# Performance work log

Measured on AMD Instinct MI355X. Metric: run time of the kernel, lower is better.

The kernel has to match this reference:

```python
import jax, jax.numpy as jnp
import numpy as np
from jax import lax

EPS = 1e-12


def _conv_block(x, w, scale, bias, pool):
    # x: (N, Cin, H, W), w: (Cout, Cin, 3, 3). BN in eval mode folded into scale/bias.
    y = lax.conv_general_dilated(x, w, window_strides=(1, 1), padding='SAME',
                                 dimension_numbers=('NCHW', 'OIHW', 'NCHW'))
    y = y * scale[None, :, None, None] + bias[None, :, None, None]
    y = jax.nn.relu(y)
    if pool:
        y = lax.reduce_window(y, -jnp.inf, lax.max, (1, 1, 2, 2), (1, 1, 2, 2), 'VALID')
    return y


def _encoder(x, w1, s1, b1, w2, s2, b2, w3, s3, b3, w4, s4, b4):
    x = _conv_block(x, w1, s1, b1, True)
    x = _conv_block(x, w2, s2, b2, True)
    x = _conv_block(x, w3, s3, b3, False)
    x = _conv_block(x, w4, s4, b4, False)
    return x  # (N, 64, 21, 21)


def _l2norm(x, axis):
    n = jnp.sqrt(jnp.sum(x * x, axis=axis, keepdims=True))
    return x / jnp.maximum(n, EPS)


def setup_inputs() -> dict:
    key = jax.random.key(0)
    ks = jax.random.split(key, 8)
    B, NQ, Way, Shot, C, H, W = 2, 75, 5, 5, 3, 84, 84
    D = 64
    inp = {
        'query': jax.random.normal(ks[0], (B, NQ, C, H, W), jnp.float32),
        'support': jax.random.normal(ks[1], (B, Way, Shot, C, H, W), jnp.float32),
        'w1': jax.random.normal(ks[2], (D, C, 3, 3), jnp.float32) * 0.1,
        'w2': jax.random.normal(ks[3], (D, D, 3, 3), jnp.float32) * 0.05,
        'w3': jax.random.normal(ks[4], (D, D, 3, 3), jnp.float32) * 0.05,
        'w4': jax.random.normal(ks[5], (D, D, 3, 3), jnp.float32) * 0.05,
    }
    for i in range(1, 5):
        inp[f's{i}'] = jnp.ones((D,), jnp.float32)
        inp[f'b{i}'] = jnp.zeros((D,), jnp.float32)
    return inp


def reference(query, support, w1, s1, b1, w2, s2, b2, w3, s3, b3, w4, s4, b4):
    B, NQ, C, H, W = query.shape
    _, Way, Shot, _, _, _ = support.shape
    q_flat = query.reshape(B * NQ, C, H, W)
    s_flat = support.reshape(B * Way * Shot, C, H, W)
    q_feat = _encoder(q_flat, w1, s1, b1, w2, s2, b2, w3, s3, b3, w4, s4, b4)
    s_feat = _encoder(s_flat, w1, s1, b1, w2, s2, b2, w3, s3, b3, w4, s4, b4)
    D, h, w = q_feat.shape[1], q_feat.shape[2], q_feat.shape[3]
    HW = h * w
    q_local = _l2norm(q_feat.reshape(B, NQ, D, HW), axis=2)            # (B,NQ,D,HW)
    s_local = s_feat.reshape(B, Way, Shot, D, HW).mean(axis=2)          # mean over shots
    s_local = _l2norm(s_local, axis=2)                                  # (B,Way,D,HW)
    # all pairwise local cosine similarities, batched in one einsum
    sim = jnp.einsum('bqdm,bcdn->bqcmn', q_local, s_local)              # (B,NQ,Way,HW,HW)
    best = sim.max(axis=-1)                                             # best match per query descriptor
    scores = best.mean(axis=-1)                                         # (B,NQ,Way)
    return scores.reshape(B * NQ, Way)
```

## Files before the change

kernel.cpp:

```cpp
#include <hip/hip_runtime.h>

#define EPS 1e-12f

#define NIMG   200
#define NQIMG  150
#define BDIM   2
#define NQ     75
#define WAY    5
#define SHOT   5
#define DCH    64
#define H1     84
#define H2     42
#define H3     21
#define HW1    7056
#define HW2    1764
#define HW3    441
#define PH     86
#define PSZ    7396
#define SST    448

#define PAD_BLKS  17335
#define W1_BLKS   8
#define W_BLKS    432

typedef __attribute__((ext_vector_type(8))) short bf16x8;
typedef __attribute__((ext_vector_type(4))) float f32x4;

__device__ __forceinline__ unsigned short f2bf(float f) {
    unsigned u = __float_as_uint(f);
    u += 0x7fffu + ((u >> 16) & 1u);
    return (unsigned short)(u >> 16);
}
__device__ __forceinline__ float bf2f(unsigned short h) {
    return __uint_as_float(((unsigned)h) << 16);
}
__device__ __forceinline__ int swz(int pix, int c) {
    return pix * 128 + ((c ^ ((pix >> 1) & 7)) << 4);
}

__global__ __launch_bounds__(256) void prep(
    const float* __restrict__ qin, const float* __restrict__ sin_,
    const float* __restrict__ w1, const float* __restrict__ s1,
    const float* __restrict__ w2, const float* __restrict__ s2,
    const float* __restrict__ w3, const float* __restrict__ s3,
    const float* __restrict__ w4, const float* __restrict__ s4,
    unsigned short* __restrict__ pad, unsigned short* __restrict__ p1,
    unsigned short* __restrict__ p2, unsigned short* __restrict__ p3,
    unsigned short* __restrict__ p4)
{
    int blk = blockIdx.x;
    if (blk < PAD_BLKS) {
        int idx = blk * 256 + threadIdx.x;
        if (idx >= NIMG * 3 * PSZ) return;
        int img = idx / (3 * PSZ);
        int rem = idx % (3 * PSZ);
        int ci = rem / PSZ, p = rem % PSZ;
        int iy = p / PH, ix = p % PH;
        float v = 0.f;
        if (iy >= 1 && iy <= H1 && ix >= 1 && ix <= H1) {
            const float* src = (img < NQIMG) ? (qin + (size_t)img * 3 * HW1)
                                             : (sin_ + (size_t)(img - NQIMG) * 3 * HW1);
            v = src[(size_t)ci * HW1 + (iy - 1) * H1 + (ix - 1)];
        }
        pad[idx] = f2bf(v);
    } else if (blk < PAD_BLKS + W1_BLKS) {
        int idx = (blk - PAD_BLKS) * 256 + threadIdx.x;
        int j = idx & 7, lane = (idx >> 3) & 63, mt = idx >> 9;
        int co = (mt << 4) + (lane & 15);
        int k = ((lane >> 4) << 3) + j;
        float v = 0.f;
        if (k < 27) {
            int ci = k / 9, s = k % 9;
            v = w1[(co * 3 + ci) * 9 + s] * s1[co];
        }
        p1[idx] = f2bf(v);
    } else {
        int idx = (blk - PAD_BLKS - W1_BLKS) * 256 + threadIdx.x;
        int which = idx / 36864;
        int r = idx % 36864;
        int j = r & 7, lane = (r >> 3) & 63, mt = (r >> 9) & 3, t = (r >> 11) & 1, s = r >> 12;
        int co = (mt << 4) + (lane & 15);
        int ci = (t << 5) + ((lane >> 4) << 3) + j;
        const float* w = (which == 0) ? w2 : (which == 1) ? w3 : w4;
        const float* sc = (which == 0) ? s2 : (which == 1) ? s3 : s4;
        unsigned short* p = (which == 0) ? p2 : (which == 1) ? p3 : p4;
        p[r] = f2bf(w[(co * 64 + ci) * 9 + s] * sc[co]);
    }
}

__global__ __launch_bounds__(256) void conv1_mfma(
    const unsigned short* __restrict__ pad,
    const unsigned short* __restrict__ wp1,
    const float* __restrict__ bias,
    unsigned short* __restrict__ out)
{
    int img = blockIdx.x / 7, seg = blockIdx.x % 7;
    int tid = threadIdx.x;
    __shared__ unsigned short strip[3 * 14 * 86];

    const unsigned* srcd = (const unsigned*)pad;
    size_t ibase = (size_t)img * 3 * (PSZ / 2);
    #pragma unroll
    for (int it = 0; it < 8; it++) {
        int i = it * 256 + tid;
        if (i < 1806) {
            int ci = i / 602, r = i % 602;
            ((unsigned*)strip)[i] = srcd[ibase + ci * (PSZ / 2) + 516 * seg + r];
        }
    }
    __syncthreads();

    int wv = tid >> 6, lane = tid & 63;
    int lc = lane & 15, kg = lane >> 4;

    const bf16x8* wvv = (const bf16x8*)wp1;
    bf16x8 a0 = wvv[lane];
    bf16x8 a1 = wvv[64 + lane];
    bf16x8 a2 = wvv[128 + lane];
    bf16x8 a3 = wvv[192 + lane];

    int off[8];
    #pragma unroll
    for (int j = 0; j < 8; j++) {
        int k = (kg << 3) + j;
        int kk = k < 27 ? k : 0;
        int ci = kk / 9, s = kk % 9;
        off[j] = ci * 1204 + (s / 3) * 86 + (s % 3);
    }

    f32x4 bini[4];
    #pragma unroll
    for (int mt = 0; mt < 4; mt++) {
        float4 bq = *reinterpret_cast<const float4*>(bias + (mt << 4) + (kg << 2));
        bini[mt] = (f32x4){bq.x, bq.y, bq.z, bq.w};
    }

    #pragma unroll
    for (int it = 0; it < 4; it++) {
        int pl = it * 64 + wv * 16 + lc;
        bool valid = pl < 252;
        int plc = valid ? pl : 251;
        int pyl = plc / 42, pxl = plc % 42;
        int base = pyl * 172 + 2 * pxl;

        bf16x8 b[4];
        #pragma unroll
        for (int j = 0; j < 8; j++) {
            int a = base + off[j];
            b[0][j] = (short)strip[a];
            b[1][j] = (short)strip[a + 1];
            b[2][j] = (short)strip[a + 86];
            b[3][j] = (short)strip[a + 87];
        }

        f32x4 acc[4][4];
        #pragma unroll
        for (int mt = 0; mt < 4; mt++)
            #pragma unroll
            for (int sub = 0; sub < 4; sub++)
                acc[mt][sub] = bini[mt];
        #pragma unroll
        for (int sub = 0; sub < 4; sub++) {
            acc[0][sub] = __builtin_amdgcn_mfma_f32_16x16x32_bf16(a0, b[sub], acc[0][sub], 0, 0, 0);
            acc[1][sub] = __builtin_amdgcn_mfma_f32_16x16x32_bf16(a1, b[sub], acc[1][sub], 0, 0, 0);
            acc[2][sub] = __builtin_amdgcn_mfma_f32_16x16x32_bf16(a2, b[sub], acc[2][sub], 0, 0, 0);
            acc[3][sub] = __builtin_amdgcn_mfma_f32_16x16x32_bf16(a3, b[sub], acc[3][sub], 0, 0, 0);
        }

        if (valid) {
            int p = seg * 252 + pl;
            #pragma unroll
            for (int mt = 0; mt < 4; mt++) {
                unsigned short uo[4];
                #pragma unroll
                for (int r = 0; r < 4; r++) {
                    float m = fmaxf(fmaxf(acc[mt][0][r], acc[mt][1][r]),
                                    fmaxf(acc[mt][2][r], acc[mt][3][r]));
                    uo[r] = f2bf(fmaxf(m, 0.f));
                }
                uint2 pk;
                pk.x = (unsigned)uo[0] | ((unsigned)uo[1] << 16);
                pk.y = (unsigned)uo[2] | ((unsigned)uo[3] << 16);
                *reinterpret_cast<uint2*>(out + ((size_t)img * HW2 + p) * DCH + (mt << 4) + (kg << 2)) = pk;
            }
        }
    }
}

__global__ __launch_bounds__(256) void conv2_mfma_pool(
    const unsigned short* __restrict__ act,
    const unsigned short* __restrict__ wp,
    const float* __restrict__ bias,
    unsigned short* __restrict__ out)
{
    int img = blockIdx.x / 7, tg = blockIdx.x % 7;
    int tid = threadIdx.x;
    __shared__ unsigned short lds[8 * 44 * DCH];

    const unsigned short* ab = act + (size_t)img * HW2 * DCH;
    int ybase = 6 * tg - 1;
    #pragma unroll
    for (int it = 0; it < 11; it++) {
        int idx = it * 256 + tid;
        int pix = idx >> 3, c = idx & 7;
        int r = pix / 44, xx = pix % 44;
        int y = ybase + r, x = xx - 1;
        bf16x8 v = (bf16x8)(short)0;
        if ((unsigned)y < (unsigned)H2 && (unsigned)x < (unsigned)H2)
            v = *(const bf16x8*)(ab + ((size_t)(y * H2 + x)) * DCH + (c << 3));
        *(bf16x8*)((char*)lds + swz(pix, c)) = v;
    }
    __syncthreads();

    int wv = tid >> 6, lane = tid & 63;
    int lc = lane & 15, kg = lane >> 4;
    int p_local = wv * 16 + lc;
    bool valid = p_local < 63;
    int pl = valid ? p_local : 62;
    int pyl = pl / 21, pxl = pl % 21;
    int pixc[4];
    #pragma unroll
    for (int sub = 0; sub < 4; sub++)
        pixc[sub] = (2 * pyl + (sub >> 1) + 1) * 44 + (2 * pxl + (sub & 1) + 1);

    f32x4 bini[4];
    #pragma unroll
    for (int mt = 0; mt < 4; mt++) {
        float4 bq = *reinterpret_cast<const float4*>(bias + (mt << 4) + (kg << 2));
        bini[mt] = (f32x4){bq.x, bq.y, bq.z, bq.w};
    }

    const bf16x8* wvv = (const bf16x8*)wp;
    f32x4 acc[4][4];
    #pragma unroll
    for (int i = 0; i < 4; i++)
        #pragma unroll
        for (int j = 0; j < 4; j++)
            acc[i][j] = bini[i];

    for (int s = 0; s < 9; s++) {
        int offs = (s / 3 - 1) * 44 + (s % 3 - 1);
        #pragma unroll
        for (int t = 0; t < 2; t++) {
            int fbase = ((s * 2 + t) * 4) << 6;
            bf16x8 a0 = wvv[fbase + lane];
            bf16x8 a1 = wvv[fbase + 64 + lane];
            bf16x8 a2 = wvv[fbase + 128 + lane];
            bf16x8 a3 = wvv[fbase + 192 + lane];
            int c = (t << 2) + kg;
            bf16x8 b[4];
            #pragma unroll
            for (int sub = 0; sub < 4; sub++) {
                int pix = pixc[sub] + offs;
                b[sub] = *(const bf16x8*)((const char*)lds + swz(pix, c));
            }
            #pragma unroll
            for (int sub = 0; sub < 4; sub++) {
                acc[0][sub] = __builtin_amdgcn_mfma_f32_16x16x32_bf16(a0, b[sub], acc[0][sub], 0, 0, 0);
                acc[1][sub] = __builtin_amdgcn_mfma_f32_16x16x32_bf16(a1, b[sub], acc[1][sub], 0, 0, 0);
                acc[2][sub] = __builtin_amdgcn_mfma_f32_16x16x32_bf16(a2, b[sub], acc[2][sub], 0, 0, 0);
                acc[3][sub] = __builtin_amdgcn_mfma_f32_16x16x32_bf16(a3, b[sub], acc[3][sub], 0, 0, 0);
            }
        }
    }

    if (!valid) return;
    int p = tg * 63 + p_local;
    #pragma unroll
    for (int mt = 0; mt < 4; mt++) {
        unsigned short uo[4];
        #pragma unroll
        for (int r = 0; r < 4; r++) {
            float m = fmaxf(fmaxf(acc[mt][0][r], acc[mt][1][r]),
                            fmaxf(acc[mt][2][r], acc[mt][3][r]));
            uo[r] = f2bf(fmaxf(m, 0.f));
        }
        uint2 pk;
        pk.x = (unsigned)uo[0] | ((unsigned)uo[1] << 16);
        pk.y = (unsigned)uo[2] | ((unsigned)uo[3] << 16);
        *reinterpret_cast<uint2*>(out + ((size_t)img * HW3 + p) * DCH + (mt << 4) + (kg << 2)) = pk;
    }
}

__global__ __launch_bounds__(256) void conv34_fused(
    const unsigned short* __restrict__ act,
    const unsigned short* __restrict__ wp3, const unsigned short* __restrict__ wp4,
    const float* __restrict__ b3, const float* __restrict__ b4,
    unsigned short* __restrict__ a4out,
    unsigned short* __restrict__ qlout)
{
    int img = blockIdx.x;
    int tid = threadIdx.x;
    __shared__ unsigned short lds[529 * DCH];

    const unsigned short* ab = act + (size_t)img * HW3 * DCH;
    #pragma unroll
    for (int it = 0; it < 17; it++) {
        int idx = it * 256 + tid;
        if (idx < 529 * 8) {
            int pix = idx >> 3, c = idx & 7;
            int r = pix / 23, xx = pix % 23;
            int y = r - 1, x = xx - 1;
            bf16x8 v = (bf16x8)(short)0;
            if ((unsigned)y < (unsigned)H3 && (unsigned)x < (unsigned)H3)
                v = *(const bf16x8*)(ab + ((size_t)(y * H3 + x)) * DCH + (c << 3));
            *(bf16x8*)((char*)lds + swz(pix, c)) = v;
        }
    }
    __syncthreads();

    int wv = tid >> 6, lane = tid & 63;
    int lc = lane & 15, kg = lane >> 4;
    int pixBase[7];
    bool pv[7];
    #pragma unroll
    for (int i = 0; i < 7; i++) {
        int p = (wv * 7 + i) * 16 + lc;
        pv[i] = p < HW3;
        int pc = pv[i] ? p : HW3 - 1;
        pixBase[i] = (pc / 21) * 23 + (pc % 21);
    }

    f32x4 bini[4];
    #pragma unroll
    for (int mt = 0; mt < 4; mt++) {
        float4 bq = *reinterpret_cast<const float4*>(b3 + (mt << 4) + (kg << 2));
        bini[mt] = (f32x4){bq.x, bq.y, bq.z, bq.w};
    }

    f32x4 acc[7][4];
    #pragma unroll
    for (int i = 0; i < 7; i++)
        #pragma unroll
        for (int m = 0; m < 4; m++)
            acc[i][m] = bini[m];

    const bf16x8* wv3 = (const bf16x8*)wp3;
    for (int s = 0; s < 9; s++) {
        int offs = (s / 3) * 23 + (s % 3);
        #pragma unroll
        for (int t = 0; t < 2; t++) {
            int fbase = ((s * 2 + t) * 4) << 6;
            bf16x8 a0 = wv3[fbase + lane];
            bf16x8 a1 = wv3[fbase + 64 + lane];
            bf16x8 a2 = wv3[fbase + 128 + lane];
            bf16x8 a3 = wv3[fbase + 192 + lane];
            int c = (t << 2) + kg;
            #pragma unroll
            for (int i = 0; i < 7; i++) {
                int pix = pixBase[i] + offs;
                bf16x8 bb = *(const bf16x8*)((const char*)lds + swz(pix, c));
                acc[i][0] = __builtin_amdgcn_mfma_f32_16x16x32_bf16(a0, bb, acc[i][0], 0, 0, 0);
                acc[i][1] = __builtin_amdgcn_mfma_f32_16x16x32_bf16(a1, bb, acc[i][1], 0, 0, 0);
                acc[i][2] = __builtin_amdgcn_mfma_f32_16x16x32_bf16(a2, bb, acc[i][2], 0, 0, 0);
                acc[i][3] = __builtin_amdgcn_mfma_f32_16x16x32_bf16(a3, bb, acc[i][3], 0, 0, 0);
            }
        }
    }

    __syncthreads();

    #pragma unroll
    for (int i = 0; i < 7; i++) {
        if (!pv[i]) continue;
        int pix = pixBase[i] + 24;
        #pragma unroll
        for (int mt = 0; mt < 4; mt++) {
            unsigned short uo[4];
            #pragma unroll
            for (int r = 0; r < 4; r++)
                uo[r] = f2bf(fmaxf(acc[i][mt][r], 0.f));
            uint2 pk;
            pk.x = (unsigned)uo[0] | ((unsigned)uo[1] << 16);
            pk.y = (unsigned)uo[2] | ((unsigned)uo[3] << 16);
            int c = (mt << 1) + (kg >> 1);
            *(uint2*)((char*)lds + swz(pix, c) + ((kg & 1) << 3)) = pk;
        }
    }
    #pragma unroll
    for (int it = 0; it < 3; it++) {
        int idx = it * 256 + tid;
        if (idx < 704) {
            int j = idx >> 3, c = idx & 7;
            int pix;
            if (j < 23)      pix = j;
            else if (j < 46) pix = 506 + (j - 23);
            else { int k = j - 46; pix = (1 + (k >> 1)) * 23 + (k & 1) * 22; }
            *(bf16x8*)((char*)lds + swz(pix, c)) = (bf16x8)(short)0;
        }
    }
    __syncthreads();

    #pragma unroll
    for (int mt = 0; mt < 4; mt++) {
        float4 bq = *reinterpret_cast<const float4*>(b4 + (mt << 4) + (kg << 2));
        bini[mt] = (f32x4){bq.x, bq.y, bq.z, bq.w};
    }
    #pragma unroll
    for (int i = 0; i < 7; i++)
        #pragma unroll
        for (int m = 0; m < 4; m++)
            acc[i][m] = bini[m];

    const bf16x8* wv4 = (const bf16x8*)wp4;
    for (int s = 0; s < 9; s++) {
        int offs = (s / 3) * 23 + (s % 3);
        #pragma unroll
        for (int t = 0; t < 2; t++) {
            int fbase = ((s * 2 + t) * 4) << 6;
            bf16x8 a0 = wv4[fbase + lane];
            bf16x8 a1 = wv4[fbase + 64 + lane];
            bf16x8 a2 = wv4[fbase + 128 + lane];
            bf16x8 a3 = wv4[fbase + 192 + lane];
            int c = (t << 2) + kg;
            #pragma unroll
            for (int i = 0; i < 7; i++) {
                int pix = pixBase[i] + offs;
                bf16x8 bb = *(const bf16x8*)((const char*)lds + swz(pix, c));
                acc[i][0] = __builtin_amdgcn_mfma_f32_16x16x32_bf16(a0, bb, acc[i][0], 0, 0, 0);
                acc[i][1] = __builtin_amdgcn_mfma_f32_16x16x32_bf16(a1, bb, acc[i][1], 0, 0, 0);
                acc[i][2] = __builtin_amdgcn_mfma_f32_16x16x32_bf16(a2, bb, acc[i][2], 0, 0, 0);
                acc[i][3] = __builtin_amdgcn_mfma_f32_16x16x32_bf16(a3, bb, acc[i][3], 0, 0, 0);
            }
        }
    }

    if (img < NQIMG) {
        #pragma unroll
        for (int i = 0; i < 7; i++) {
            float v[4][4];
            float ssq = 0.f;
            #pragma unroll
            for (int mt = 0; mt < 4; mt++)
                #pragma unroll
                for (int r = 0; r < 4; r++) {
                    float x = fmaxf(acc[i][mt][r], 0.f);
                    v[mt][r] = x;
                    ssq = fmaf(x, x, ssq);
                }
            ssq += __shfl_xor(ssq, 16, 64);
            ssq += __shfl_xor(ssq, 32, 64);
            float inv = 1.f / fmaxf(sqrtf(ssq), EPS);
            if (!pv[i]) continue;
            int p = (wv * 7 + i) * 16 + lc;
            #pragma unroll
            for (int mt = 0; mt < 4; mt++) {
                unsigned short uo[4];
                #pragma unroll
                for (int r = 0; r < 4; r++)
                    uo[r] = f2bf(v[mt][r] * inv);
                uint2 pk;
                pk.x = (unsigned)uo[0] | ((unsigned)uo[1] << 16);
                pk.y = (unsigned)uo[2] | ((unsigned)uo[3] << 16);
                *reinterpret_cast<uint2*>(qlout + ((size_t)img * HW3 + p) * DCH + (mt << 4) + (kg << 2)) = pk;
            }
        }
    } else {
        #pragma unroll
        for (int mt = 0; mt < 4; mt++) {
            #pragma unroll
            for (int i = 0; i < 7; i++) {
                if (!pv[i]) continue;
                int p = (wv * 7 + i) * 16 + lc;
                unsigned short uo[4];
                #pragma unroll
                for (int r = 0; r < 4; r++)
                    uo[r] = f2bf(fmaxf(acc[i][mt][r], 0.f));
                uint2 pk;
                pk.x = (unsigned)uo[0] | ((unsigned)uo[1] << 16);
                pk.y = (unsigned)uo[2] | ((unsigned)uo[3] << 16);
                *reinterpret_cast<uint2*>(a4out + ((size_t)img * HW3 + p) * DCH + (mt << 4) + (kg << 2)) = pk;
            }
        }
    }
}

__global__ __launch_bounds__(256) void s_mean_norm(
    const unsigned short* __restrict__ feat, unsigned short* __restrict__ s_local)
{
    int idx = blockIdx.x * 256 + threadIdx.x;
    if (idx >= BDIM * WAY * SST) return;
    int hw = idx % SST;
    int bc = idx / SST;
    bf16x8* o = (bf16x8*)(s_local + (size_t)idx * DCH);
    if (hw >= HW3) {
        #pragma unroll
        for (int g = 0; g < 8; g++) o[g] = (bf16x8)(short)0;
        return;
    }
    int img0 = NQIMG + bc * SHOT;
    float v[DCH];
    #pragma unroll
    for (int d = 0; d < DCH; d++) v[d] = 0.f;
    for (int sh = 0; sh < SHOT; sh++) {
        const bf16x8* f = (const bf16x8*)(feat + ((size_t)(img0 + sh) * HW3 + hw) * DCH);
        #pragma unroll
        for (int g = 0; g < 8; g++) {
            bf16x8 x = f[g];
            #pragma unroll
            for (int j = 0; j < 8; j++)
                v[g * 8 + j] += bf2f((unsigned short)x[j]);
        }
    }
    float ss = 0.f;
    #pragma unroll
    for (int d = 0; d < DCH; d++) {
        v[d] *= (1.f / SHOT);
        ss = fmaf(v[d], v[d], ss);
    }
    float inv = 1.f / fmaxf(sqrtf(ss), EPS);
    #pragma unroll
    for (int g = 0; g < 8; g++) {
        bf16x8 pk;
        #pragma unroll
        for (int j = 0; j < 8; j++) pk[j] = (short)f2bf(v[g * 8 + j] * inv);
        o[g] = pk;
    }
}

__global__ __launch_bounds__(256) void sim_mfma(
    const unsigned short* __restrict__ qloc,
    const unsigned short* __restrict__ sloc,
    float* __restrict__ out)
{
    int blk = blockIdx.x;
    int imgq = blk / WAY, way = blk % WAY;
    int b = imgq / NQ;
    const unsigned short* qp = qloc + (size_t)imgq * HW3 * DCH;
    const unsigned short* sp = sloc + (size_t)(b * WAY + way) * SST * DCH;

    int tid = threadIdx.x;
    int wv = tid >> 6, lane = tid & 63;
    int lc = lane & 15, kg = lane >> 4;
    int mt0 = wv * 7;

    bf16x8 qa0[7], qa1[7];
    #pragma unroll
    for (int i = 0; i < 7; i++) {
        const unsigned short* qrow = qp + (size_t)((mt0 + i) * 16 + lc) * DCH + (kg << 3);
        qa0[i] = *(const bf16x8*)(qrow);
        qa1[i] = *(const bf16x8*)(qrow + 32);
    }
    f32x4 rmax[7];
    #pragma unroll
    for (int i = 0; i < 7; i++)
        rmax[i] = (f32x4){-1e30f, -1e30f, -1e30f, -1e30f};

    const f32x4 z4 = (f32x4){0.f, 0.f, 0.f, 0.f};
    const unsigned short* sbase = sp + (size_t)lc * DCH + (kg << 3);

    #pragma unroll
    for (int g = 0; g < 6; g++) {
        bf16x8 s0[4], s1[4];
        #pragma unroll
        for (int u = 0; u < 4; u++) {
            const unsigned short* r0 = sbase + (size_t)(4 * g + u) * 16 * DCH;
            s0[u] = *(const bf16x8*)(r0);
            s1[u] = *(const bf16x8*)(r0 + 32);
        }
        #pragma unroll
        for (int i = 0; i < 7; i++) {
            f32x4 a[4];
            #pragma unroll
            for (int u = 0; u < 4; u++) {
                a[u] = __builtin_amdgcn_mfma_f32_16x16x32_bf16(qa0[i], s0[u], z4, 0, 0, 0);
                a[u] = __builtin_amdgcn_mfma_f32_16x16x32_bf16(qa1[i], s1[u], a[u], 0, 0, 0);
            }
            #pragma unroll
            for (int r = 0; r < 4; r++) {
                float t = fmaxf(fmaxf(rmax[i][r], a[0][r]), a[1][r]);
                rmax[i][r] = fmaxf(fmaxf(t, a[2][r]), a[3][r]);
            }
        }
    }
    {
        bf16x8 s0[4], s1[4];
        #pragma unroll
        for (int u = 0; u < 4; u++) {
            const unsigned short* r0 = sbase + (size_t)(24 + u) * 16 * DCH;
            s0[u] = *(const bf16x8*)(r0);
            s1[u] = *(const bf16x8*)(r0 + 32);
        }
        bool nval = (432 + lc) < HW3;
        #pragma unroll
        for (int i = 0; i < 7; i++) {
            f32x4 a[4];
            #pragma unroll
            for (int u = 0; u < 4; u++) {
                a[u] = __builtin_amdgcn_mfma_f32_16x16x32_bf16(qa0[i], s0[u], z4, 0, 0, 0);
                a[u] = __builtin_amdgcn_mfma_f32_16x16x32_bf16(qa1[i], s1[u], a[u], 0, 0, 0);
            }
            #pragma unroll
            for (int r = 0; r < 4; r++) {
                float t = fmaxf(fmaxf(rmax[i][r], a[0][r]), a[1][r]);
                rmax[i][r] = fmaxf(fmaxf(t, a[2][r]), nval ? a[3][r] : -1e30f);
            }
        }
    }

    float msum = 0.f;
    #pragma unroll
    for (int i = 0; i < 7; i++) {
        #pragma unroll
        for (int r = 0; r < 4; r++) {
            float v = rmax[i][r];
            v = fmaxf(v, __shfl_xor(v, 1, 64));
            v = fmaxf(v, __shfl_xor(v, 2, 64));
            v = fmaxf(v, __shfl_xor(v, 4, 64));
            v = fmaxf(v, __shfl_xor(v, 8, 64));
            int m = (mt0 + i) * 16 + (kg << 2) + r;
            if (lc == 0 && m < HW3) msum += v;
        }
    }
    #pragma unroll
    for (int off = 32; off > 0; off >>= 1)
        msum += __shfl_xor(msum, off, 64);
    __shared__ float red[4];
    if (lane == 0) red[wv] = msum;
    __syncthreads();
    if (tid == 0)
        out[(size_t)imgq * WAY + way] = (red[0] + red[1] + red[2] + red[3]) * (1.f / HW3);
}

extern "C" void kernel_launch(void* const* d_in, const int* in_sizes, int n_in,
                              void* d_out, int out_size, void* d_ws, size_t ws_size,
                              hipStream_t stream) {
    const float* query   = (const float*)d_in[0];
    const float* support = (const float*)d_in[1];
    const float* w1 = (const float*)d_in[2];
    const float* w2 = (const float*)d_in[3];
    const float* w3 = (const float*)d_in[4];
    const float* w4 = (const float*)d_in[5];
    const float* s1 = (const float*)d_in[6];
    const float* b1 = (const float*)d_in[7];
    const float* s2 = (const float*)d_in[8];
    const float* b2 = (const float*)d_in[9];
    const float* s3 = (const float*)d_in[10];
    const float* b3 = (const float*)d_in[11];
    const float* s4 = (const float*)d_in[12];
    const float* b4 = (const float*)d_in[13];
    float* out = (float*)d_out;

    char* ws = (char*)d_ws;
    unsigned short* A1  = (unsigned short*)(ws);
    unsigned short* A2  = (unsigned short*)(ws + 45158400);
    unsigned short* A4  = (unsigned short*)(ws + 56448000);
    unsigned short* QL  = (unsigned short*)(ws + 67737600);
    unsigned short* SL  = (unsigned short*)(ws + 76204800);
    unsigned short* WP2 = (unsigned short*)(ws + 76778240);
    unsigned short* WP3 = (unsigned short*)(ws + 76851968);
    unsigned short* WP4 = (unsigned short*)(ws + 76925696);
    unsigned short* WP1 = (unsigned short*)(ws + 76999424);
    unsigned short* PAD = (unsigned short*)(ws + 77003520);

    prep<<<PAD_BLKS + W1_BLKS + W_BLKS, 256, 0, stream>>>(
        query, support, w1, s1, w2, s2, w3, s3, w4, s4, PAD, WP1, WP2, WP3, WP4);

    conv1_mfma<<<NIMG * 7, 256, 0, stream>>>(PAD, WP1, b1, A1);
    conv2_mfma_pool<<<NIMG * 7, 256, 0, stream>>>(A1, WP2, b2, A2);
    conv34_fused<<<NIMG, 256, 0, stream>>>(A2, WP3, WP4, b3, b4, A4, QL);

    s_mean_norm<<<(BDIM * WAY * SST + 255) / 256, 256, 0, stream>>>(A4, SL);

    sim_mfma<<<NQIMG * WAY, 256, 0, stream>>>(QL, SL, out);
}
```

Baseline: 137.2 us.

## Stage support descriptors in swizzled LDS for sim kernel; vectorize input padding

The similarity kernel now copies each block's support descriptor tile (448x64 bf16) into XOR-swizzled shared memory once, and all four waves read their MFMA B-operands from LDS instead of each issuing redundant global loads. Separately, the input padding/bf16-conversion step in the prep kernel now handles four elements per thread and writes them with one 8-byte store, cutting the block count by four. The LDS staging adds a barrier and about 57KB of shared memory per block, which may limit occupancy.

Measured after the change: 126.4 us, median of 3. -7.8%, faster.

```diff
diff --git a/kernel.cpp b/kernel.cpp
--- a/kernel.cpp
+++ b/kernel.cpp
@@ -19,7 +19,7 @@
 #define PSZ    7396
 #define SST    448
 
-#define PAD_BLKS  17335
+#define PAD_BLKS  4334
 #define W1_BLKS   8
 #define W_BLKS    432
 
@@ -50,19 +50,28 @@
 {
     int blk = blockIdx.x;
     if (blk < PAD_BLKS) {
-        int idx = blk * 256 + threadIdx.x;
-        if (idx >= NIMG * 3 * PSZ) return;
+        int idx4 = blk * 256 + threadIdx.x;
+        if (idx4 >= NIMG * 3 * PSZ / 4) return;
+        int idx = idx4 * 4;
         int img = idx / (3 * PSZ);
         int rem = idx % (3 * PSZ);
         int ci = rem / PSZ, p = rem % PSZ;
-        int iy = p / PH, ix = p % PH;
-        float v = 0.f;
-        if (iy >= 1 && iy <= H1 && ix >= 1 && ix <= H1) {
-            const float* src = (img < NQIMG) ? (qin + (size_t)img * 3 * HW1)
-                                             : (sin_ + (size_t)(img - NQIMG) * 3 * HW1);
-            v = src[(size_t)ci * HW1 + (iy - 1) * H1 + (ix - 1)];
-        }
-        pad[idx] = f2bf(v);
+        const float* src = (img < NQIMG) ? (qin + (size_t)img * 3 * HW1)
+                                         : (sin_ + (size_t)(img - NQIMG) * 3 * HW1);
+        unsigned short o[4];
+        #pragma unroll
+        for (int e = 0; e < 4; e++) {
+            int pe = p + e;
+            int iy = pe / PH, ix = pe % PH;
+            float v = 0.f;
+            if (iy >= 1 && iy <= H1 && ix >= 1 && ix <= H1)
+                v = src[(size_t)ci * HW1 + (iy - 1) * H1 + (ix - 1)];
+            o[e] = f2bf(v);
+        }
+        uint2 pk;
+        pk.x = (unsigned)o[0] | ((unsigned)o[1] << 16);
+        pk.y = (unsigned)o[2] | ((unsigned)o[3] << 16);
+        *reinterpret_cast<uint2*>(pad + idx) = pk;
     } else if (blk < PAD_BLKS + W1_BLKS) {
         int idx = (blk - PAD_BLKS) * 256 + threadIdx.x;
         int j = idx & 7, lane = (idx >> 3) & 63, mt = idx >> 9;
@@ -529,7 +538,17 @@
     const unsigned short* qp = qloc + (size_t)imgq * HW3 * DCH;
     const unsigned short* sp = sloc + (size_t)(b * WAY + way) * SST * DCH;
 
+    __shared__ unsigned short slds[SST * DCH];
     int tid = threadIdx.x;
+    #pragma unroll
+    for (int it = 0; it < 14; it++) {
+        int idx = it * 256 + tid;
+        int pix = idx >> 3, c = idx & 7;
+        bf16x8 v = *(const bf16x8*)(sp + ((size_t)pix << 6) + (c << 3));
+        *(bf16x8*)((char*)slds + swz(pix, c)) = v;
+    }
+    __syncthreads();
+
     int wv = tid >> 6, lane = tid & 63;
     int lc = lane & 15, kg = lane >> 4;
     int mt0 = wv * 7;
@@ -547,16 +566,15 @@
         rmax[i] = (f32x4){-1e30f, -1e30f, -1e30f, -1e30f};
 
     const f32x4 z4 = (f32x4){0.f, 0.f, 0.f, 0.f};
-    const unsigned short* sbase = sp + (size_t)lc * DCH + (kg << 3);
 
     #pragma unroll
     for (int g = 0; g < 6; g++) {
         bf16x8 s0[4], s1[4];
         #pragma unroll
         for (int u = 0; u < 4; u++) {
-            const unsigned short* r0 = sbase + (size_t)(4 * g + u) * 16 * DCH;
-            s0[u] = *(const bf16x8*)(r0);
-            s1[u] = *(const bf16x8*)(r0 + 32);
+            int pix = (4 * g + u) * 16 + lc;
+            s0[u] = *(const bf16x8*)((const char*)slds + swz(pix, kg));
+            s1[u] = *(const bf16x8*)((const char*)slds + swz(pix, 4 + kg));
         }
         #pragma unroll
         for (int i = 0; i < 7; i++) {
@@ -577,9 +595,9 @@
         bf16x8 s0[4], s1[4];
         #pragma unroll
         for (int u = 0; u < 4; u++) {
-            const unsigned short* r0 = sbase + (size_t)(24 + u) * 16 * DCH;
-            s0[u] = *(const bf16x8*)(r0);
-            s1[u] = *(const bf16x8*)(r0 + 32);
+            int pix = (24 + u) * 16 + lc;
+            s0[u] = *(const bf16x8*)((const char*)slds + swz(pix, kg));
+            s1[u] = *(const bf16x8*)((const char*)slds + swz(pix, 4 + kg));
         }
         bool nval = (432 + lc) < HW3;
         #pragma unroll
```
